# Kernel tuning notes

Hardware: AMD Instinct MI355X
Metric: run time of the kernel (lower is better)

Reference implementation:

```python
import jax, jax.numpy as jnp
import numpy as np

S, SM, B, D, H, NHEAD = 1024, 1024, 4, 1024, 2048, 16
EPS = 1e-5


def layer_norm(x, g, b):
    mu = jnp.mean(x, axis=-1, keepdims=True)
    var = jnp.var(x, axis=-1, keepdims=True)
    return (x - mu) * jax.lax.rsqrt(var + EPS) * g + b


def mha(q_in, k_in, v_in, w_in, b_in, w_out, b_out):
    # q_in: [Sq,B,D], k_in/v_in: [Sk,B,D]; torch nn.MultiheadAttention math (eval)
    Sq, Bn, Dn = q_in.shape
    Sk = k_in.shape[0]
    hd = Dn // NHEAD
    wq, wk, wv = jnp.split(w_in, 3, axis=0)
    bq, bk, bv = jnp.split(b_in, 3)
    q = (q_in @ wq.T + bq) * (hd ** -0.5)
    k = k_in @ wk.T + bk
    v = v_in @ wv.T + bv
    rs = lambda x, L: x.reshape(L, Bn, NHEAD, hd).transpose(1, 2, 0, 3)  # [B,h,L,hd]
    qh, kh, vh = rs(q, Sq), rs(k, Sk), rs(v, Sk)
    att = jax.nn.softmax(jnp.einsum('bhqd,bhkd->bhqk', qh, kh), axis=-1)
    o = jnp.einsum('bhqk,bhkd->bhqd', att, vh).transpose(2, 0, 1, 3).reshape(Sq, Bn, Dn)
    return o @ w_out.T + b_out


def sru(x, w, v, b):
    # SRU cell with input projection (n_in != n_out -> k=4): candidate, f, r, highway
    Ssz, Bsz, _ = x.shape
    U = (x @ w).reshape(Ssz, Bsz, 4, H)  # [S,B,4,H]
    vf, vr = v[0], v[1]
    bf, br = b[0], b[1]

    def step(c, u):
        xc, fp, rp, xh = u[:, 0], u[:, 1], u[:, 2], u[:, 3]
        f = jax.nn.sigmoid(fp + vf * c + bf)
        r = jax.nn.sigmoid(rp + vr * c + br)
        c2 = f * c + (1.0 - f) * xc
        h = r * c2 + (1.0 - r) * xh
        return c2, h

    c0 = jnp.zeros((Bsz, H), x.dtype)
    _, hs = jax.lax.scan(step, c0, U)
    return hs  # [S,B,H]


def setup_inputs():
    key = jax.random.key(0)
    ks = jax.random.split(key, 12)
    n = lambda k, shp, sc=0.02: jax.random.normal(k, shp, dtype=jnp.float32) * sc
    return dict(
        tgt=n(ks[0], (S, B, D), 1.0),
        memory=n(ks[1], (SM, B, D), 1.0),
        sa_w_in=n(ks[2], (3 * D, D)), sa_b_in=jnp.zeros((3 * D,)),
        sa_w_out=n(ks[3], (D, D)), sa_b_out=jnp.zeros((D,)),
        ca_w_in=n(ks[4], (3 * D, D)), ca_b_in=jnp.zeros((3 * D,)),
        ca_w_out=n(ks[5], (D, D)), ca_b_out=jnp.zeros((D,)),
        sru_w=n(ks[6], (D, 4 * H)), sru_v=n(ks[7], (2, H)), sru_b=jnp.zeros((2, H)),
        lin2_w=n(ks[8], (D, H)), lin2_b=jnp.zeros((D,)),
        ln1_g=jnp.ones((D,)), ln1_b=jnp.zeros((D,)),
        ln2_g=jnp.ones((D,)), ln2_b=jnp.zeros((D,)),
        ln3_g=jnp.ones((D,)), ln3_b=jnp.zeros((D,)),
    )


def reference(tgt, memory, sa_w_in, sa_b_in, sa_w_out, sa_b_out,
              ca_w_in, ca_b_in, ca_w_out, ca_b_out,
              sru_w, sru_v, sru_b, lin2_w, lin2_b,
              ln1_g, ln1_b, ln2_g, ln2_b, ln3_g, ln3_b):
    # dropout layers are identity in eval mode
    t2 = mha(tgt, tgt, tgt, sa_w_in, sa_b_in, sa_w_out, sa_b_out)
    t = layer_norm(tgt + t2, ln1_g, ln1_b)
    t2 = mha(t, memory, memory, ca_w_in, ca_b_in, ca_w_out, ca_b_out)
    t = layer_norm(t + t2, ln2_g, ln2_b)
    h = sru(t, sru_w, sru_v, sru_b)
    t2 = h @ lin2_w.T + lin2_b
    t = layer_norm(t + t2, ln3_g, ln3_b)
    return t
```

## Files before the change

kernel.cpp:

```cpp
#include <hip/hip_runtime.h>
#include <hip/hip_bf16.h>

typedef __bf16 bf16;
typedef bf16 bf16x8 __attribute__((ext_vector_type(8)));
typedef bf16 bf16x4 __attribute__((ext_vector_type(4)));
typedef float f32x4 __attribute__((ext_vector_type(4)));

#define MFMA16(a, b, c) __builtin_amdgcn_mfma_f32_16x16x32_bf16((a), (b), (c), 0, 0, 0)

__device__ __forceinline__ void gl_lds16(const void* g, void* l) {
    __builtin_amdgcn_global_load_lds((const __attribute__((address_space(1))) void*)g,
                                     (__attribute__((address_space(3))) void*)l, 16, 0, 0);
}

__global__ __launch_bounds__(256) void k_detect(const void* __restrict__ src, int* __restrict__ flag) {
    __shared__ int cnt;
    if (threadIdx.x == 0) cnt = 0;
    __syncthreads();
    const unsigned int* w = (const unsigned int*)src;
    int local = 0;
    for (int i = threadIdx.x; i < 4096; i += 256) {
        unsigned int e = (w[i] >> 7) & 0xFF;
        local += (e > 100 && e < 150) ? 1 : 0;
    }
    atomicAdd(&cnt, local);
    __syncthreads();
    if (threadIdx.x == 0) *flag = (cnt > 2048) ? 1 : 0;
}

struct BigSegs {
    const void* src[6];
    bf16* dst[6];
    int cum[7];
};
__global__ __launch_bounds__(256) void k_norm_big(const int* __restrict__ flag, BigSegs s) {
    int seg = 0;
#pragma unroll
    for (int t = 0; t < 5; t++) seg += (blockIdx.x >= s.cum[t + 1]) ? 1 : 0;
    int i = (blockIdx.x - s.cum[seg]) * 256 + threadIdx.x;
    const void* sp = s.src[seg];
    bf16* dp = s.dst[seg];
    if (*flag) {
        ((bf16x8*)dp)[i] = ((const bf16x8*)sp)[i];
    } else {
        const float* fs = (const float*)sp + (size_t)i * 8;
        bf16x8 o;
#pragma unroll
        for (int j = 0; j < 8; j++) o[j] = (bf16)fs[j];
        ((bf16x8*)dp)[i] = o;
    }
}

struct SmallSegs {
    const void* src[13];
    bf16* dst[13];
    int n8[13];
};
__global__ __launch_bounds__(256) void k_norm_multi(const int* __restrict__ flag, SmallSegs s) {
    int seg = blockIdx.x;
    const void* sp = s.src[seg];
    bf16* dp = s.dst[seg];
    int n = s.n8[seg];
    int f = *flag;
    for (int i = threadIdx.x; i < n; i += 256) {
        if (f) {
            ((bf16x8*)dp)[i] = ((const bf16x8*)sp)[i];
        } else {
            const float* fs = (const float*)sp + (size_t)i * 8;
            bf16x8 o;
#pragma unroll
            for (int j = 0; j < 8; j++) o[j] = (bf16)fs[j];
            ((bf16x8*)dp)[i] = o;
        }
    }
}

__global__ __launch_bounds__(256) void k_cvt(const int* __restrict__ flag, const void* __restrict__ in,
                                             bf16* __restrict__ outb) {
    size_t i = (size_t)blockIdx.x * 256 + threadIdx.x;
    bf16x8 v;
    if (*flag) {
        v = ((const bf16x8*)in)[i];
    } else {
        f32x4 a = ((const f32x4*)in)[i * 2];
        f32x4 b = ((const f32x4*)in)[i * 2 + 1];
#pragma unroll
        for (int j = 0; j < 4; j++) { v[j] = (bf16)a[j]; v[4 + j] = (bf16)b[j]; }
    }
    ((bf16x8*)outb)[i] = v;
}

__global__ __launch_bounds__(256) void k_transpose(const int* __restrict__ flag, const void* __restrict__ in,
                                                   bf16* __restrict__ out, int R, int C) {
    __shared__ __align__(16) bf16 t[64][72];
    int tid = threadIdx.x;
    int c0 = blockIdx.x * 64, r0 = blockIdx.y * 64;
#pragma unroll
    for (int i = 0; i < 2; i++) {
        int idx = tid + i * 256;
        int r = idx >> 3, ch = idx & 7;
        size_t base = (size_t)(r0 + r) * C + c0 + ch * 8;
        bf16x8 v;
        if (*flag) {
            v = *(const bf16x8*)((const bf16*)in + base);
        } else {
            const float* f = (const float*)in + base;
            f32x4 x = *(const f32x4*)f, y = *(const f32x4*)(f + 4);
#pragma unroll
            for (int j = 0; j < 4; j++) { v[j] = (bf16)x[j]; v[4 + j] = (bf16)y[j]; }
        }
        *(bf16x8*)&t[r][ch * 8] = v;
    }
    __syncthreads();
    int nbase = c0 & 2047, joff = c0 >> 11;
#pragma unroll
    for (int i = 0; i < 2; i++) {
        int idx = tid + i * 256;
        int cr = idx >> 3, ch = idx & 7;
        bf16x8 v;
#pragma unroll
        for (int j = 0; j < 8; j++) v[j] = t[ch * 8 + j][cr];
        int np = (nbase + cr) * 4 + joff;
        *(bf16x8*)(out + (size_t)np * R + r0 + ch * 8) = v;
    }
}

__global__ __launch_bounds__(256) void k_vtr(const bf16* __restrict__ in, int ldv, bf16* __restrict__ out) {
    int nt = blockIdx.x, st = blockIdx.y, b = blockIdx.z;
    __shared__ __align__(16) bf16 t[64][72];
    int tid = threadIdx.x;
#pragma unroll
    for (int i = 0; i < 2; i++) {
        int idx = tid + i * 256;
        int r = idx >> 3, ch = idx & 7;
        bf16x8 v = *(const bf16x8*)(in + (size_t)((st * 64 + r) * 4 + b) * ldv + nt * 64 + ch * 8);
        *(bf16x8*)&t[r][ch * 8] = v;
    }
    __syncthreads();
#pragma unroll
    for (int i = 0; i < 2; i++) {
        int idx = tid + i * 256;
        int dr = idx >> 3, ch = idx & 7;
        bf16x8 v;
#pragma unroll
        for (int j = 0; j < 8; j++) v[j] = t[ch * 8 + j][dr];
        *(bf16x8*)(out + (size_t)(b * 1024 + nt * 64 + dr) * 1024 + st * 64 + ch * 8) = v;
    }
}

__device__ __forceinline__ int swzB(int r, int byteInRow) {
    return r * 128 + (byteInRow ^ ((r & 7) << 4));
}

template <int BM, bool USCAT>
__global__ __launch_bounds__(256) void k_gemm(
    const bf16* __restrict__ A, int lda,
    const bf16* __restrict__ W, int ldw,
    const bf16* __restrict__ bias,
    float* __restrict__ Cf, bf16* __restrict__ Cb, int ldc,
    int K, int scale_end, float scale) {
    constexpr int MI = BM / 32;
    __shared__ __align__(16) char Asm[BM * 128];
    __shared__ __align__(16) char Bsm[128 * 128];
    int tid = threadIdx.x, w = tid >> 6, l = tid & 63, lg = l >> 4, lm = l & 15;
    int wm = w >> 1, wn = w & 1;
    int m0 = blockIdx.y * BM, n0 = blockIdx.x * 128;

    f32x4 acc[MI][4] = {};

    for (int k0 = 0; k0 < K; k0 += 64) {
#pragma unroll
        for (int i = 0; i < BM / 32; i++) {
            int r = i * 32 + w * 8 + (l >> 3);
            int gs = (l & 7) ^ (r & 7);
            gl_lds16(A + (size_t)(m0 + r) * lda + k0 + gs * 8,
                     Asm + (i * 32 + w * 8) * 128);
        }
#pragma unroll
        for (int i = 0; i < 4; i++) {
            int r = i * 32 + w * 8 + (l >> 3);
            int gs = (l & 7) ^ (r & 7);
            gl_lds16(W + (size_t)(n0 + r) * ldw + k0 + gs * 8,
                     Bsm + (i * 32 + w * 8) * 128);
        }
        __syncthreads();
#pragma unroll
        for (int kh = 0; kh < 2; kh++) {
            bf16x8 af[MI], bfr[4];
#pragma unroll
            for (int i = 0; i < MI; i++)
                af[i] = *(const bf16x8*)(Asm + swzB(wm * (BM / 2) + i * 16 + lm, kh * 64 + lg * 16));
#pragma unroll
            for (int j = 0; j < 4; j++)
                bfr[j] = *(const bf16x8*)(Bsm + swzB(wn * 64 + j * 16 + lm, kh * 64 + lg * 16));
#pragma unroll
            for (int i = 0; i < MI; i++)
#pragma unroll
                for (int j = 0; j < 4; j++)
                    acc[i][j] = MFMA16(af[i], bfr[j], acc[i][j]);
        }
        __syncthreads();
    }
    if constexpr (USCAT) {
        bf16* lsA = (bf16*)Asm;
        bf16* lsB = (bf16*)Bsm;
#pragma unroll
        for (int j = 0; j < 4; j++) {
            int cl = wn * 16 + j * 4 + (lm >> 2);
            int g = lm & 3;
            bf16* ls = (g < 2) ? lsA : lsB;
            int g01 = g & 1;
#pragma unroll
            for (int i = 0; i < MI; i++) {
                int slb = wm * 16 + i * 4 + lg;
                int boff = (slb * 2 + g01) * 2;
                int swz = boff ^ ((cl & 7) << 4);
#pragma unroll
                for (int r = 0; r < 4; r++) {
                    float v = acc[i][j][r];
                    *(bf16*)((char*)ls + (r * 32 + cl) * 128 + swz) = (bf16)v;
                }
            }
        }
        __syncthreads();
        int buf = tid >> 7, bb = (tid >> 5) & 3, cl = tid & 31;
        const char* ls = (buf == 0) ? (const char*)lsA : (const char*)lsB;
        bf16* dstbase = (buf == 0) ? Cb : (bf16*)Cf;
        int ch = bb * 2048 + (n0 >> 2) + cl;
        size_t gbase = (size_t)ch * 2048 + (size_t)(m0 >> 2) * 2;
        const char* src = ls + (bb * 32 + cl) * 128;
#pragma unroll
        for (int q = 0; q < 8; q++) {
            int pq = (q * 16) ^ ((cl & 7) << 4);
            *(bf16x8*)(dstbase + gbase + q * 8) = *(const bf16x8*)(src + pq);
        }
    } else {
#pragma unroll
        for (int j = 0; j < 4; j++) {
            int col = n0 + wn * 64 + j * 16 + lm;
            float bv = bias ? (float)bias[col] : 0.f;
            float sc = (col < scale_end) ? scale : 1.f;
#pragma unroll
            for (int i = 0; i < MI; i++) {
                int row = m0 + wm * (BM / 2) + i * 16 + lg * 4;
#pragma unroll
                for (int r = 0; r < 4; r++) {
                    float v = (acc[i][j][r] + bv) * sc;
                    size_t idx = (size_t)(row + r) * ldc + col;
                    if (Cf) Cf[idx] = v;
                    if (Cb) Cb[idx] = (bf16)v;
                }
            }
        }
    }
}

__device__ __forceinline__ int swz2(int row, int byteInRow) {
    return row * 128 + (byteInRow ^ ((row & 7) << 4));
}
__device__ __forceinline__ int swzP(int row, int byteInRow) {
    return row * 128 + (byteInRow ^ ((row & 3) << 4) ^ (((row >> 2) & 1) << 6));
}

__global__ __launch_bounds__(256) void k_attn(
    const bf16* __restrict__ Qp, const bf16* __restrict__ Kp, const bf16* __restrict__ Vt,
    int ldq, int ldk, bf16* __restrict__ Op) {
    int h = blockIdx.x & 15, b = blockIdx.x >> 4, qblk = blockIdx.y;
    int tid = threadIdx.x, w = tid >> 6, l = tid & 63, lg = l >> 4, lm = l & 15;
    int r0 = tid >> 3, ch = tid & 7;

    __shared__ __align__(16) char Ksm[64 * 128];
    __shared__ __align__(16) char Vsm[64 * 128];
    __shared__ __align__(16) char Psm[4][32 * 128];

    bf16x8 qf[2][2];
#pragma unroll
    for (int u = 0; u < 2; u++) {
        int qrow = qblk * 128 + w * 32 + u * 16 + lm;
#pragma unroll
        for (int kk = 0; kk < 2; kk++)
            qf[u][kk] = *(const bf16x8*)(Qp + (size_t)(qrow * 4 + b) * ldq + h * 64 + kk * 32 + lg * 8);
    }

    const bf16* vbase = Vt + (size_t)(b * 1024 + h * 64) * 1024;

    bf16x8 kreg[2], vreg[2];
#pragma unroll
    for (int p = 0; p < 2; p++) {
        int r = r0 + p * 32;
        kreg[p] = *(const bf16x8*)(Kp + (size_t)(r * 4 + b) * ldk + h * 64 + ch * 8);
        vreg[p] = *(const bf16x8*)(vbase + (size_t)r * 1024 + ch * 8);
    }

    f32x4 oa[2][4] = {};
    float mrun[2][4], lrun[2][4];
#pragma unroll
    for (int u = 0; u < 2; u++)
#pragma unroll
        for (int r = 0; r < 4; r++) { mrun[u][r] = -1e30f; lrun[u][r] = 0.f; }

    for (int kt = 0; kt < 16; kt++) {
        __syncthreads();
#pragma unroll
        for (int p = 0; p < 2; p++) {
            int r = r0 + p * 32;
            *(bf16x8*)(Ksm + swz2(r, ch * 16)) = kreg[p];
            *(bf16x8*)(Vsm + swz2(r, ch * 16)) = vreg[p];
        }
        if (kt < 15) {
#pragma unroll
            for (int p = 0; p < 2; p++) {
                int r = (kt + 1) * 64 + r0 + p * 32;
                kreg[p] = *(const bf16x8*)(Kp + (size_t)(r * 4 + b) * ldk + h * 64 + ch * 8);
                vreg[p] = *(const bf16x8*)(vbase + (size_t)(r0 + p * 32) * 1024 + (kt + 1) * 64 + ch * 8);
            }
        }
        __syncthreads();

        f32x4 sc[2][4] = {};
#pragma unroll
        for (int kk = 0; kk < 2; kk++)
#pragma unroll
            for (int jt = 0; jt < 4; jt++) {
                bf16x8 bk = *(const bf16x8*)(Ksm + swz2(jt * 16 + lm, kk * 64 + lg * 16));
#pragma unroll
                for (int u = 0; u < 2; u++)
                    sc[u][jt] = MFMA16(qf[u][kk], bk, sc[u][jt]);
            }

        float lmax[2][4];
        bool grow = false;
#pragma unroll
        for (int u = 0; u < 2; u++)
#pragma unroll
            for (int r = 0; r < 4; r++) {
                lmax[u][r] = fmaxf(fmaxf(sc[u][0][r], sc[u][1][r]), fmaxf(sc[u][2][r], sc[u][3][r]));
                grow = grow || (lmax[u][r] > mrun[u][r] + 8.f);
            }
        if (__any(grow)) {
#pragma unroll
            for (int u = 0; u < 2; u++)
#pragma unroll
                for (int r = 0; r < 4; r++) {
                    float m = lmax[u][r];
#pragma unroll
                    for (int d = 1; d < 16; d <<= 1) m = fmaxf(m, __shfl_xor(m, d));
                    float mn = fmaxf(mrun[u][r], m);
                    float al = __expf(mrun[u][r] - mn);
                    mrun[u][r] = mn;
                    lrun[u][r] *= al;
#pragma unroll
                    for (int ot = 0; ot < 4; ot++) oa[u][ot][r] *= al;
                }
        }
#pragma unroll
        for (int u = 0; u < 2; u++)
#pragma unroll
            for (int jt = 0; jt < 4; jt++)
#pragma unroll
                for (int r = 0; r < 4; r++) {
                    float p = __expf(sc[u][jt][r] - mrun[u][r]);
                    sc[u][jt][r] = p;
                    lrun[u][r] += p;
                }
#pragma unroll
        for (int u = 0; u < 2; u++)
#pragma unroll
            for (int jt = 0; jt < 4; jt++)
#pragma unroll
                for (int r = 0; r < 4; r++)
                    *(bf16*)(Psm[w] + swzP(u * 16 + lg * 4 + r, (jt * 16 + lm) * 2)) = (bf16)sc[u][jt][r];
        asm volatile("s_waitcnt lgkmcnt(0)" ::: "memory");
        __builtin_amdgcn_sched_barrier(0);
#pragma unroll
        for (int kk = 0; kk < 2; kk++) {
            bf16x8 pa[2];
#pragma unroll
            for (int u = 0; u < 2; u++)
                pa[u] = *(const bf16x8*)(Psm[w] + swzP(u * 16 + lm, kk * 64 + lg * 16));
#pragma unroll
            for (int ot = 0; ot < 4; ot++) {
                bf16x8 bv = *(const bf16x8*)(Vsm + swz2(ot * 16 + lm, kk * 64 + lg * 16));
#pragma unroll
                for (int u = 0; u < 2; u++)
                    oa[u][ot] = MFMA16(pa[u], bv, oa[u][ot]);
            }
        }
    }
#pragma unroll
    for (int u = 0; u < 2; u++)
#pragma unroll
        for (int r = 0; r < 4; r++) {
#pragma unroll
            for (int d = 1; d < 16; d <<= 1) lrun[u][r] += __shfl_xor(lrun[u][r], d);
            float inv = 1.f / lrun[u][r];
            int srow = qblk * 128 + w * 32 + u * 16 + lg * 4 + r;
#pragma unroll
            for (int ot = 0; ot < 4; ot++) {
                int col = h * 64 + ot * 16 + lm;
                Op[(size_t)(srow * 4 + b) * 1024 + col] = (bf16)(oa[u][ot][r] * inv);
            }
        }
}

template <typename XT>
__global__ __launch_bounds__(256) void k_addln(
    const XT* __restrict__ X, const float* __restrict__ Yd,
    const bf16* __restrict__ g, const bf16* __restrict__ bb,
    float* __restrict__ outF, bf16* __restrict__ outB) {
    int row = blockIdx.x * 4 + (threadIdx.x >> 6);
    int l = threadIdx.x & 63;
    const XT* xr = X + (size_t)row * 1024;
    const float* yr = Yd + (size_t)row * 1024;
    float v[16];
    float s = 0.f, s2 = 0.f;
#pragma unroll
    for (int q = 0; q < 4; q++) {
        float xa[4];
        if constexpr (sizeof(XT) == 4) {
            f32x4 a = *(const f32x4*)(xr + l * 4 + q * 256);
#pragma unroll
            for (int j = 0; j < 4; j++) xa[j] = a[j];
        } else {
            bf16x4 a = *(const bf16x4*)(xr + l * 4 + q * 256);
#pragma unroll
            for (int j = 0; j < 4; j++) xa[j] = (float)a[j];
        }
        f32x4 c = *(const f32x4*)(yr + l * 4 + q * 256);
#pragma unroll
        for (int j = 0; j < 4; j++) {
            float t = xa[j] + c[j];
            v[q * 4 + j] = t;
            s += t;
            s2 += t * t;
        }
    }
#pragma unroll
    for (int d = 1; d < 64; d <<= 1) { s += __shfl_xor(s, d); s2 += __shfl_xor(s2, d); }
    float mu = s * (1.f / 1024.f);
    float var = s2 * (1.f / 1024.f) - mu * mu;
    float rstd = rsqrtf(var + 1e-5f);
#pragma unroll
    for (int q = 0; q < 4; q++)
#pragma unroll
        for (int j = 0; j < 4; j++) {
            int col = l * 4 + q * 256 + j;
            float y = (v[q * 4 + j] - mu) * rstd * (float)g[col] + (float)bb[col];
            if (outF) outF[(size_t)row * 1024 + col] = y;
            if (outB) outB[(size_t)row * 1024 + col] = (bf16)y;
        }
}

__global__ __launch_bounds__(64) void k_sru_ab(
    const bf16* __restrict__ U2a, const bf16* __restrict__ v2, const bf16* __restrict__ b2,
    float* __restrict__ AB) {
    int ch = blockIdx.x * 64 + threadIdx.x;
    int g = blockIdx.y;
    int hh = ch & 2047;
    float vf = (float)v2[hh], bfv = (float)b2[hh];
    const bf16x8* u = (const bf16x8*)(U2a + (size_t)ch * 2048 + g * 256);
    float A = 1.f, c = 0.f;
    bf16x8 q[4];
#pragma unroll
    for (int i = 0; i < 4; i++) q[i] = u[i];
    for (int it = 0; it < 8; it++) {
#pragma unroll
        for (int j = 0; j < 4; j++) {
            int cidx = it * 4 + j;
            bf16x8 v = q[j];
            if (cidx + 4 < 32) q[j] = u[cidx + 4];
#pragma unroll
            for (int t = 0; t < 4; t++) {
                float xc = (float)v[t * 2], fp = (float)v[t * 2 + 1];
                float f = 1.f / (1.f + __expf(-(fp + vf * c + bfv)));
                A *= f;
                c = f * c + (1.f - f) * xc;
            }
        }
    }
    AB[(size_t)(g * 8192 + ch) * 2] = A;
    AB[(size_t)(g * 8192 + ch) * 2 + 1] = c;
}

__global__ __launch_bounds__(64) void k_sru_h(
    const bf16* __restrict__ U2a, const bf16* __restrict__ U2b,
    const bf16* __restrict__ v2, const bf16* __restrict__ b2,
    const float* __restrict__ AB, bf16* __restrict__ Hb) {
    int ch = blockIdx.x * 64 + threadIdx.x;
    int g = blockIdx.y;
    int b = ch >> 11, hh = ch & 2047;
    float vf = (float)v2[hh], vr = (float)v2[2048 + hh];
    float bfv = (float)b2[hh], brv = (float)b2[2048 + hh];
    float c = 0.f;
    for (int s = 0; s < g; s++) {
        float As = AB[(size_t)(s * 8192 + ch) * 2];
        float Bs = AB[(size_t)(s * 8192 + ch) * 2 + 1];
        c = As * c + Bs;
    }
    const bf16x8* ua = (const bf16x8*)(U2a + (size_t)ch * 2048 + g * 256);
    const bf16x8* ub = (const bf16x8*)(U2b + (size_t)ch * 2048 + g * 256);
    bf16* ho = Hb + ((size_t)(g * 128) * 4 + b) * 2048 + hh;
    bf16x8 qa[4], qb[4];
#pragma unroll
    for (int i = 0; i < 4; i++) { qa[i] = ua[i]; qb[i] = ub[i]; }
    for (int it = 0; it < 8; it++) {
#pragma unroll
        for (int j = 0; j < 4; j++) {
            int cidx = it * 4 + j;
            bf16x8 va = qa[j], vb = qb[j];
            if (cidx + 4 < 32) { qa[j] = ua[cidx + 4]; qb[j] = ub[cidx + 4]; }
#pragma unroll
            for (int t = 0; t < 4; t++) {
                float xc = (float)va[t * 2], fp = (float)va[t * 2 + 1];
                float rp = (float)vb[t * 2], xh = (float)vb[t * 2 + 1];
                float f = 1.f / (1.f + __expf(-(fp + vf * c + bfv)));
                float r = 1.f / (1.f + __expf(-(rp + vr * c + brv)));
                c = f * c + (1.f - f) * xc;
                float hv = r * c + (1.f - r) * xh;
                ho[(size_t)(cidx * 4 + t) * 8192] = (bf16)hv;
            }
        }
    }
}

extern "C" void kernel_launch(void* const* d_in, const int* in_sizes, int n_in,
                              void* d_out, int out_size, void* d_ws, size_t ws_size,
                              hipStream_t stream) {
    const size_t MB = 1u << 20;
    char* ws = (char*)d_ws;

    bf16* memB    = (bf16*)(ws + 0);
    bf16* sawinB  = (bf16*)(ws + 8 * MB);
    bf16* sawoutB = (bf16*)(ws + 14 * MB);
    bf16* cawinB  = (bf16*)(ws + 16 * MB);
    bf16* cawoutB = (bf16*)(ws + 22 * MB);
    bf16* lin2wB  = (bf16*)(ws + 24 * MB);
    char* S0 = ws + 28 * MB;
    bf16* sabinB  = (bf16*)(S0 + 0 * 8192);
    bf16* cabinB  = (bf16*)(S0 + 1 * 8192);
    bf16* saboutB = (bf16*)(S0 + 2 * 8192);
    bf16* caboutB = (bf16*)(S0 + 3 * 8192);
    bf16* lin2bB  = (bf16*)(S0 + 4 * 8192);
    bf16* sruvB   = (bf16*)(S0 + 5 * 8192);
    bf16* srubB   = (bf16*)(S0 + 6 * 8192);
    bf16* ln1gB   = (bf16*)(S0 + 7 * 8192);
    bf16* ln1bB   = (bf16*)(S0 + 8 * 8192);
    bf16* ln2gB   = (bf16*)(S0 + 9 * 8192);
    bf16* ln2bB   = (bf16*)(S0 + 10 * 8192);
    bf16* ln3gB   = (bf16*)(S0 + 11 * 8192);
    bf16* ln3bB   = (bf16*)(S0 + 12 * 8192);
    int*  flag    = (int*)(S0 + 13 * 8192);
    float* AB     = (float*)(S0 + 128 * 1024);

    char* P = ws + 29 * MB;
    bf16*  t0b  = (bf16*)(P + 0);
    bf16*  qkv  = (bf16*)(P + 16 * MB);
    bf16*  qca  = qkv;
    bf16*  kvca = (bf16*)(P + 24 * MB);
    bf16*  obuf = (bf16*)(P + 40 * MB);
    bf16*  Vt   = (bf16*)(P + 56 * MB);
    float* tmp  = (float*)(P + 64 * MB);
    bf16*  t1   = (bf16*)(P + 80 * MB);
    bf16*  t2   = (bf16*)(ws + 0);
    bf16*  wT   = (bf16*)(P + 0);
    bf16*  U2a  = (bf16*)(P + 16 * MB);
    bf16*  U2b  = (bf16*)(P + 48 * MB);
    bf16*  hb   = (bf16*)(P + 80 * MB);
    float* tmp2 = (float*)(P + 16 * MB);

    k_detect<<<1, 256, 0, stream>>>(d_in[0], flag);
    BigSegs bg;
    {
        const void* bsrc[6] = {d_in[1], d_in[2], d_in[4], d_in[6], d_in[8], d_in[13]};
        bf16* bdst[6] = {memB, sawinB, sawoutB, cawinB, cawoutB, lin2wB};
        const int cum[7] = {0, 2048, 3584, 4096, 5632, 6144, 7168};
        for (int i = 0; i < 6; i++) { bg.src[i] = bsrc[i]; bg.dst[i] = bdst[i]; }
        for (int i = 0; i < 7; i++) bg.cum[i] = cum[i];
    }
    k_norm_big<<<7168, 256, 0, stream>>>(flag, bg);
    SmallSegs sg;
    const int srcIdx[13] = {3, 7, 5, 9, 14, 11, 12, 15, 16, 17, 18, 19, 20};
    bf16* dsts[13] = {sabinB, cabinB, saboutB, caboutB, lin2bB, sruvB, srubB,
                      ln1gB, ln1bB, ln2gB, ln2bB, ln3gB, ln3bB};
    const int n8s[13] = {384, 384, 128, 128, 128, 512, 512, 128, 128, 128, 128, 128, 128};
    for (int i = 0; i < 13; i++) { sg.src[i] = d_in[srcIdx[i]]; sg.dst[i] = dsts[i]; sg.n8[i] = n8s[i]; }
    k_norm_multi<<<13, 256, 0, stream>>>(flag, sg);

    k_cvt<<<2048, 256, 0, stream>>>(flag, d_in[0], t0b);

    k_gemm<128, false><<<dim3(24, 32), 256, 0, stream>>>(t0b, 1024, sawinB, 1024, sabinB,
                                                         nullptr, qkv, 3072, 1024, 1024, 0.125f);
    k_vtr<<<dim3(16, 16, 4), 256, 0, stream>>>(qkv + 2048, 3072, Vt);
    k_attn<<<dim3(64, 8), 256, 0, stream>>>(qkv, qkv + 1024, Vt, 3072, 3072, obuf);
    k_gemm<64, false><<<dim3(8, 64), 256, 0, stream>>>(obuf, 1024, sawoutB, 1024, saboutB,
                                                       tmp, nullptr, 1024, 1024, 0, 1.f);
    k_addln<bf16><<<1024, 256, 0, stream>>>(t0b, tmp, ln1gB, ln1bB, nullptr, t1);

    k_gemm<64, false><<<dim3(8, 64), 256, 0, stream>>>(t1, 1024, cawinB, 1024, cabinB,
                                                       nullptr, qca, 1024, 1024, 1024, 0.125f);
    k_gemm<128, false><<<dim3(16, 32), 256, 0, stream>>>(memB, 1024, cawinB + (size_t)1024 * 1024, 1024,
                                                         cabinB + 1024, nullptr, kvca, 2048, 1024, 0, 1.f);
    k_vtr<<<dim3(16, 16, 4), 256, 0, stream>>>(kvca + 1024, 2048, Vt);
    k_attn<<<dim3(64, 8), 256, 0, stream>>>(qca, kvca, Vt, 1024, 2048, obuf);
    k_gemm<64, false><<<dim3(8, 64), 256, 0, stream>>>(obuf, 1024, cawoutB, 1024, caboutB,
                                                       tmp, nullptr, 1024, 1024, 0, 1.f);
    k_addln<bf16><<<1024, 256, 0, stream>>>(t1, tmp, ln2gB, ln2bB, nullptr, t2);

    k_transpose<<<dim3(128, 16), 256, 0, stream>>>(flag, d_in[10], wT, 1024, 8192);
    k_gemm<128, true><<<dim3(64, 32), 256, 0, stream>>>(t2, 1024, wT, 1024,
                                                        nullptr, (float*)U2b, U2a, 0, 1024, 0, 1.f);
    k_sru_ab<<<dim3(128, 8), 64, 0, stream>>>(U2a, sruvB, srubB, AB);
    k_sru_h<<<dim3(128, 8), 64, 0, stream>>>(U2a, U2b, sruvB, srubB, AB, hb);
    k_gemm<64, false><<<dim3(8, 64), 256, 0, stream>>>(hb, 2048, lin2wB, 2048, lin2bB,
                                                       tmp2, nullptr, 1024, 2048, 0, 1.f);
    k_addln<bf16><<<1024, 256, 0, stream>>>(t2, tmp2, ln3gB, ln3bB, (float*)d_out, nullptr);
}
```

Measured before the change: 454.8 us.

## Skip bf16 input copies by reading originals directly; double-buffer K/V tiles in attention

When the detected input dtype is already bf16, the normalization and conversion kernels now exit early, and the GEMM and add-layernorm kernels read the original input pointers through alternate-pointer arguments. This removes redundant copy traffic for large weights and activations. The attention kernel also gets double-buffered K/V shared-memory tiles, so it needs one barrier per iteration instead of two. The cost is twice the K/V LDS footprint, which may reduce occupancy.

```diff
diff --git a/kernel.cpp b/kernel.cpp
--- a/kernel.cpp
+++ b/kernel.cpp
@@ -34,21 +34,16 @@
     int cum[7];
 };
 __global__ __launch_bounds__(256) void k_norm_big(const int* __restrict__ flag, BigSegs s) {
+    if (*flag) return;
     int seg = 0;
 #pragma unroll
     for (int t = 0; t < 5; t++) seg += (blockIdx.x >= s.cum[t + 1]) ? 1 : 0;
     int i = (blockIdx.x - s.cum[seg]) * 256 + threadIdx.x;
-    const void* sp = s.src[seg];
-    bf16* dp = s.dst[seg];
-    if (*flag) {
-        ((bf16x8*)dp)[i] = ((const bf16x8*)sp)[i];
-    } else {
-        const float* fs = (const float*)sp + (size_t)i * 8;
-        bf16x8 o;
-#pragma unroll
-        for (int j = 0; j < 8; j++) o[j] = (bf16)fs[j];
-        ((bf16x8*)dp)[i] = o;
-    }
+    const float* fs = (const float*)s.src[seg] + (size_t)i * 8;
+    bf16x8 o;
+#pragma unroll
+    for (int j = 0; j < 8; j++) o[j] = (bf16)fs[j];
+    ((bf16x8*)s.dst[seg])[i] = o;
 }
 
 struct SmallSegs {
@@ -77,16 +72,13 @@
 
 __global__ __launch_bounds__(256) void k_cvt(const int* __restrict__ flag, const void* __restrict__ in,
                                              bf16* __restrict__ outb) {
+    if (*flag) return;
     size_t i = (size_t)blockIdx.x * 256 + threadIdx.x;
+    f32x4 a = ((const f32x4*)in)[i * 2];
+    f32x4 b = ((const f32x4*)in)[i * 2 + 1];
     bf16x8 v;
-    if (*flag) {
-        v = ((const bf16x8*)in)[i];
-    } else {
-        f32x4 a = ((const f32x4*)in)[i * 2];
-        f32x4 b = ((const f32x4*)in)[i * 2 + 1];
-#pragma unroll
-        for (int j = 0; j < 4; j++) { v[j] = (bf16)a[j]; v[4 + j] = (bf16)b[j]; }
-    }
+#pragma unroll
+    for (int j = 0; j < 4; j++) { v[j] = (bf16)a[j]; v[4 + j] = (bf16)b[j]; }
     ((bf16x8*)outb)[i] = v;
 }
 
@@ -154,14 +146,19 @@
 
 template <int BM, bool USCAT>
 __global__ __launch_bounds__(256) void k_gemm(
-    const bf16* __restrict__ A, int lda,
-    const bf16* __restrict__ W, int ldw,
+    const int* __restrict__ flagp,
+    const bf16* __restrict__ A, const bf16* __restrict__ Aalt, int lda,
+    const bf16* __restrict__ W, const bf16* __restrict__ Walt, int ldw,
     const bf16* __restrict__ bias,
     float* __restrict__ Cf, bf16* __restrict__ Cb, int ldc,
     int K, int scale_end, float scale) {
     constexpr int MI = BM / 32;
     __shared__ __align__(16) char Asm[BM * 128];
     __shared__ __align__(16) char Bsm[128 * 128];
+    if (*flagp) {
+        if (Aalt) A = Aalt;
+        if (Walt) W = Walt;
+    }
     int tid = threadIdx.x, w = tid >> 6, l = tid & 63, lg = l >> 4, lm = l & 15;
     int wm = w >> 1, wn = w & 1;
     int m0 = blockIdx.y * BM, n0 = blockIdx.x * 128;
@@ -269,8 +266,8 @@
     int tid = threadIdx.x, w = tid >> 6, l = tid & 63, lg = l >> 4, lm = l & 15;
     int r0 = tid >> 3, ch = tid & 7;
 
-    __shared__ __align__(16) char Ksm[64 * 128];
-    __shared__ __align__(16) char Vsm[64 * 128];
+    __shared__ __align__(16) char Ksm[2][64 * 128];
+    __shared__ __align__(16) char Vsm[2][64 * 128];
     __shared__ __align__(16) char Psm[4][32 * 128];
 
     bf16x8 qf[2][2];
@@ -291,6 +288,13 @@
         kreg[p] = *(const bf16x8*)(Kp + (size_t)(r * 4 + b) * ldk + h * 64 + ch * 8);
         vreg[p] = *(const bf16x8*)(vbase + (size_t)r * 1024 + ch * 8);
     }
+#pragma unroll
+    for (int p = 0; p < 2; p++) {
+        int r = r0 + p * 32;
+        *(bf16x8*)(Ksm[0] + swz2(r, ch * 16)) = kreg[p];
+        *(bf16x8*)(Vsm[0] + swz2(r, ch * 16)) = vreg[p];
+    }
+    __syncthreads();
 
     f32x4 oa[2][4] = {};
     float mrun[2][4], lrun[2][4];
@@ -299,14 +303,8 @@
 #pragma unroll
         for (int r = 0; r < 4; r++) { mrun[u][r] = -1e30f; lrun[u][r] = 0.f; }
 
+    int cur = 0;
     for (int kt = 0; kt < 16; kt++) {
-        __syncthreads();
-#pragma unroll
-        for (int p = 0; p < 2; p++) {
-            int r = r0 + p * 32;
-            *(bf16x8*)(Ksm + swz2(r, ch * 16)) = kreg[p];
-            *(bf16x8*)(Vsm + swz2(r, ch * 16)) = vreg[p];
-        }
         if (kt < 15) {
 #pragma unroll
             for (int p = 0; p < 2; p++) {
@@ -315,14 +313,15 @@
                 vreg[p] = *(const bf16x8*)(vbase + (size_t)(r0 + p * 32) * 1024 + (kt + 1) * 64 + ch * 8);
             }
         }
-        __syncthreads();
+        const char* Kc = Ksm[cur];
+        const char* Vc = Vsm[cur];
 
         f32x4 sc[2][4] = {};
 #pragma unroll
         for (int kk = 0; kk < 2; kk++)
 #pragma unroll
             for (int jt = 0; jt < 4; jt++) {
-                bf16x8 bk = *(const bf16x8*)(Ksm + swz2(jt * 16 + lm, kk * 64 + lg * 16));
+                bf16x8 bk = *(const bf16x8*)(Kc + swz2(jt * 16 + lm, kk * 64 + lg * 16));
 #pragma unroll
                 for (int u = 0; u < 2; u++)
                     sc[u][jt] = MFMA16(qf[u][kk], bk, sc[u][jt]);
@@ -380,12 +379,24 @@
                 pa[u] = *(const bf16x8*)(Psm[w] + swzP(u * 16 + lm, kk * 64 + lg * 16));
 #pragma unroll
             for (int ot = 0; ot < 4; ot++) {
-                bf16x8 bv = *(const bf16x8*)(Vsm + swz2(ot * 16 + lm, kk * 64 + lg * 16));
+                bf16x8 bv = *(const bf16x8*)(Vc + swz2(ot * 16 + lm, kk * 64 + lg * 16));
 #pragma unroll
                 for (int u = 0; u < 2; u++)
                     oa[u][ot] = MFMA16(pa[u], bv, oa[u][ot]);
             }
         }
+        if (kt < 15) {
+            char* Kn = Ksm[cur ^ 1];
+            char* Vn = Vsm[cur ^ 1];
+#pragma unroll
+            for (int p = 0; p < 2; p++) {
+                int r = r0 + p * 32;
+                *(bf16x8*)(Kn + swz2(r, ch * 16)) = kreg[p];
+                *(bf16x8*)(Vn + swz2(r, ch * 16)) = vreg[p];
+            }
+            __syncthreads();
+        }
+        cur ^= 1;
     }
 #pragma unroll
     for (int u = 0; u < 2; u++)
@@ -405,9 +416,11 @@
 
 template <typename XT>
 __global__ __launch_bounds__(256) void k_addln(
-    const XT* __restrict__ X, const float* __restrict__ Yd,
+    const int* __restrict__ flagp,
+    const XT* __restrict__ X, const XT* __restrict__ Xalt, const float* __restrict__ Yd,
     const bf16* __restrict__ g, const bf16* __restrict__ bb,
     float* __restrict__ outF, bf16* __restrict__ outB) {
+    if (*flagp && Xalt) X = Xalt;
     int row = blockIdx.x * 4 + (threadIdx.x >> 6);
     int l = threadIdx.x & 63;
     const XT* xr = X + (size_t)row * 1024;
@@ -568,6 +581,14 @@
     bf16*  hb   = (bf16*)(P + 80 * MB);
     float* tmp2 = (float*)(P + 16 * MB);
 
+    const bf16* tgtA   = (const bf16*)d_in[0];
+    const bf16* memA   = (const bf16*)d_in[1];
+    const bf16* sawinA = (const bf16*)d_in[2];
+    const bf16* sawoutA= (const bf16*)d_in[4];
+    const bf16* cawinA = (const bf16*)d_in[6];
+    const bf16* cawoutA= (const bf16*)d_in[8];
+    const bf16* lin2wA = (const bf16*)d_in[13];
+
     k_detect<<<1, 256, 0, stream>>>(d_in[0], flag);
     BigSegs bg;
     {
@@ -588,30 +609,32 @@
 
     k_cvt<<<2048, 256, 0, stream>>>(flag, d_in[0], t0b);
 
-    k_gemm<128, false><<<dim3(24, 32), 256, 0, stream>>>(t0b, 1024, sawinB, 1024, sabinB,
-                                                         nullptr, qkv, 3072, 1024, 1024, 0.125f);
+    k_gemm<128, false><<<dim3(24, 32), 256, 0, stream>>>(flag, t0b, tgtA, 1024, sawinB, sawinA, 1024,
+                                                         sabinB, nullptr, qkv, 3072, 1024, 1024, 0.125f);
     k_vtr<<<dim3(16, 16, 4), 256, 0, stream>>>(qkv + 2048, 3072, Vt);
     k_attn<<<dim3(64, 8), 256, 0, stream>>>(qkv, qkv + 1024, Vt, 3072, 3072, obuf);
-    k_gemm<64, false><<<dim3(8, 64), 256, 0, stream>>>(obuf, 1024, sawoutB, 1024, saboutB,
-                                                       tmp, nullptr, 1024, 1024, 0, 1.f);
-    k_addln<bf16><<<1024, 256, 0, stream>>>(t0b, tmp, ln1gB, ln1bB, nullptr, t1);
-
-    k_gemm<64, false><<<dim3(8, 64), 256, 0, stream>>>(t1, 1024, cawinB, 1024, cabinB,
-                                                       nullptr, qca, 1024, 1024, 1024, 0.125f);
-    k_gemm<128, false><<<dim3(16, 32), 256, 0, stream>>>(memB, 1024, cawinB + (size_t)1024 * 1024, 1024,
+    k_gemm<64, false><<<dim3(8, 64), 256, 0, stream>>>(flag, obuf, nullptr, 1024, sawoutB, sawoutA, 1024,
+                                                       saboutB, tmp, nullptr, 1024, 1024, 0, 1.f);
+    k_addln<bf16><<<1024, 256, 0, stream>>>(flag, t0b, tgtA, tmp, ln1gB, ln1bB, nullptr, t1);
+
+    k_gemm<64, false><<<dim3(8, 64), 256, 0, stream>>>(flag, t1, nullptr, 1024, cawinB, cawinA, 1024,
+                                                       cabinB, nullptr, qca, 1024, 1024, 1024, 0.125f);
+    k_gemm<128, false><<<dim3(16, 32), 256, 0, stream>>>(flag, memB, memA, 1024,
+                                                         cawinB + (size_t)1024 * 1024,
+                                                         cawinA + (size_t)1024 * 1024, 1024,
                                                          cabinB + 1024, nullptr, kvca, 2048, 1024, 0, 1.f);
     k_vtr<<<dim3(16, 16, 4), 256, 0, stream>>>(kvca + 1024, 2048, Vt);
     k_attn<<<dim3(64, 8), 256, 0, stream>>>(qca, kvca, Vt, 1024, 2048, obuf);
-    k_gemm<64, false><<<dim3(8, 64), 256, 0, stream>>>(obuf, 1024, cawoutB, 1024, caboutB,
-                                                       tmp, nullptr, 1024, 1024, 0, 1.f);
-    k_addln<bf16><<<1024, 256, 0, stream>>>(t1, tmp, ln2gB, ln2bB, nullptr, t2);
+    k_gemm<64, false><<<dim3(8, 64), 256, 0, stream>>>(flag, obuf, nullptr, 1024, cawoutB, cawoutA, 1024,
+                                                       caboutB, tmp, nullptr, 1024, 1024, 0, 1.f);
+    k_addln<bf16><<<1024, 256, 0, stream>>>(flag, t1, nullptr, tmp, ln2gB, ln2bB, nullptr, t2);
 
     k_transpose<<<dim3(128, 16), 256, 0, stream>>>(flag, d_in[10], wT, 1024, 8192);
-    k_gemm<128, true><<<dim3(64, 32), 256, 0, stream>>>(t2, 1024, wT, 1024,
+    k_gemm<128, true><<<dim3(64, 32), 256, 0, stream>>>(flag, t2, nullptr, 1024, wT, nullptr, 1024,
                                                         nullptr, (float*)U2b, U2a, 0, 1024, 0, 1.f);
     k_sru_ab<<<dim3(128, 8), 64, 0, stream>>>(U2a, sruvB, srubB, AB);
     k_sru_h<<<dim3(128, 8), 64, 0, stream>>>(U2a, U2b, sruvB, srubB, AB, hb);
-    k_gemm<64, false><<<dim3(8, 64), 256, 0, stream>>>(hb, 2048, lin2wB, 2048, lin2bB,
-                                                       tmp2, nullptr, 1024, 2048, 0, 1.f);
-    k_addln<bf16><<<1024, 256, 0, stream>>>(t2, tmp2, ln3gB, ln3bB, (float*)d_out, nullptr);
-}
+    k_gemm<64, false><<<dim3(8, 64), 256, 0, stream>>>(flag, hb, nullptr, 2048, lin2wB, lin2wA, 2048,
+                                                       lin2bB, tmp2, nullptr, 1024, 2048, 0, 1.f);
+    k_addln<bf16><<<1024, 256, 0, stream>>>(flag, t2, nullptr, tmp2, ln3gB, ln3bB, (float*)d_out, nullptr);
+}
```

Measured after the change: 455.1 us. Within noise of the previous version (+0.1%).
